# Performance work log

Measured on AMD Instinct MI355X. Metric: run time of the kernel, lower is better.

Reference implementation:

```python
import jax, jax.numpy as jnp
import numpy as np

NUM_HEADS = 8


def setup_inputs() -> dict:
    key = jax.random.key(0)
    ks = jax.random.split(key, 9)
    B, S, E = 16, 2048, 768
    s = 0.02
    return {
        "features": jax.random.normal(ks[0], (B, S, E), jnp.float32),
        "in_proj_w": jax.random.normal(ks[1], (3 * E, E), jnp.float32) * s,
        "in_proj_b": jnp.zeros((3 * E,), jnp.float32),
        "out_proj_w": jax.random.normal(ks[2], (E, E), jnp.float32) * s,
        "out_proj_b": jnp.zeros((E,), jnp.float32),
        "w1": jax.random.normal(ks[3], (384, E), jnp.float32) * s,
        "b1": jnp.zeros((384,), jnp.float32),
        "w2": jax.random.normal(ks[4], (1, 384), jnp.float32) * s,
        "b2": jnp.zeros((1,), jnp.float32),
    }


def reference(features, in_proj_w, in_proj_b, out_proj_w, out_proj_b, w1, b1, w2, b2):
    # torch nn.MultiheadAttention default batch_first=False: dim 0 is the
    # attended sequence axis (length B here), dim 1 is the MHA batch (S).
    B, S, E = features.shape
    H = NUM_HEADS
    Dh = E // H
    qkv = features @ in_proj_w.T + in_proj_b          # (B, S, 3E)
    q, k, v = jnp.split(qkv, 3, axis=-1)
    q = q.reshape(B, S, H, Dh)
    k = k.reshape(B, S, H, Dh)
    v = v.reshape(B, S, H, Dh)
    scale = 1.0 / jnp.sqrt(jnp.asarray(Dh, features.dtype))
    # attention over axis-0 positions (l, m in 0..B-1), per (s, h)
    scores = jnp.einsum('lshd,mshd->shlm', q * scale, k)
    attn = jax.nn.softmax(scores, axis=-1)
    ctx = jnp.einsum('shlm,mshd->lshd', attn, v).reshape(B, S, E)
    attn_out = ctx @ out_proj_w.T + out_proj_b        # (B, S, E)
    # batched 2-layer MLP (replaces the Python per-row loop)
    h = jax.nn.relu(attn_out @ w1.T + b1)             # (B, S, 384)
    prob = h @ w2.T + b2                              # (B, S, 1)
    contacts = jnp.broadcast_to(prob, (B, S, S))      # contacts[:, i, :] = prob[:, i]
    return contacts
```

## Files before the change

### kernel.cpp

```cpp
#include <hip/hip_runtime.h>

typedef unsigned short u16;
typedef __attribute__((ext_vector_type(8))) __bf16 bf16x8;
typedef __attribute__((ext_vector_type(4))) float floatx4;

#define B_DIM  16
#define S_DIM  2048
#define E_DIM  768
#define HEADS  8
#define DHEAD  96
#define MROWS  32768
#define QKV_LD 2304
#define ATT_ST 392

__device__ __forceinline__ u16 f2b(float f) {
    unsigned u = __float_as_uint(f);
    u += 0x7fffu + ((u >> 16) & 1u);
    return (u16)(u >> 16);
}
__device__ __forceinline__ float blo(unsigned u) { return __uint_as_float(u << 16); }
__device__ __forceinline__ float bhi(unsigned u) { return __uint_as_float(u & 0xffff0000u); }

__device__ __forceinline__ void axpy8(float* acc, float p, uint4 v) {
    acc[0] += p * blo(v.x); acc[1] += p * bhi(v.x);
    acc[2] += p * blo(v.y); acc[3] += p * bhi(v.y);
    acc[4] += p * blo(v.z); acc[5] += p * bhi(v.z);
    acc[6] += p * blo(v.w); acc[7] += p * bhi(v.w);
}

__global__ __launch_bounds__(256) void cvt_bf16(const float* __restrict__ in,
                                                u16* __restrict__ out, int n4) {
    int i = blockIdx.x * 256 + threadIdx.x;
    if (i < n4) {
        float4 f = ((const float4*)in)[i];
        ushort4 r;
        r.x = f2b(f.x); r.y = f2b(f.y); r.z = f2b(f.z); r.w = f2b(f.w);
        ((ushort4*)out)[i] = r;
    }
}

__global__ __launch_bounds__(256) void transpose_cvt(const float* __restrict__ in,
                                                     u16* __restrict__ out) {
    __shared__ float t[32][33];
    const int tx = threadIdx.x & 31, ty = threadIdx.x >> 5;
    int x = blockIdx.x * 32 + tx;
    int y = blockIdx.y * 32 + ty;
#pragma unroll
    for (int j = 0; j < 4; j++) t[ty + j * 8][tx] = in[(long)(y + j * 8) * 768 + x];
    __syncthreads();
    x = blockIdx.y * 32 + tx;
    y = blockIdx.x * 32 + ty;
#pragma unroll
    for (int j = 0; j < 4; j++) out[(long)(y + j * 8) * 768 + x] = f2b(t[tx][ty + j * 8]);
}

__global__ __launch_bounds__(256) void cbias_kernel(const float* __restrict__ w1,
                                                    const float* __restrict__ bo,
                                                    const float* __restrict__ b1,
                                                    float* __restrict__ c) {
    __shared__ float red[4];
    const int n = blockIdx.x, tid = threadIdx.x;
    const float* row = w1 + (long)n * 768;
    float s = row[tid] * bo[tid] + row[tid + 256] * bo[tid + 256] + row[tid + 512] * bo[tid + 512];
#pragma unroll
    for (int off = 32; off > 0; off >>= 1) s += __shfl_xor(s, off);
    if ((tid & 63) == 0) red[tid >> 6] = s;
    __syncthreads();
    if (tid == 0) c[n] = red[0] + red[1] + red[2] + red[3] + b1[n];
}

template<bool OUTF32, bool PERM, bool SWIZ>
__global__ __launch_bounds__(256) void gemm_bt(const u16* __restrict__ A, int lda,
                                               const u16* __restrict__ W,
                                               const float* __restrict__ bias,
                                               void* __restrict__ Cout, int ldc,
                                               int N, int K) {
    __shared__ __align__(16) u16 sA[128 * 32];
    __shared__ __align__(16) u16 sB[128 * 32];
    const int tid  = threadIdx.x;
    int bn, bm;
    if (SWIZ) {
        const int bx = blockIdx.x;
        bn = bx >> 8;
        bm = ((bx & 7) << 5) | ((bx >> 3) & 31);
    } else {
        bn = blockIdx.x;
        bm = blockIdx.y;
    }
    const int lane = tid & 63;
    const int wid  = tid >> 6;
    const int wm   = (wid >> 1) * 64;
    const int wn   = (wid & 1) * 64;
    const int ar = tid >> 2;
    const int ac = (tid & 3) * 8;
    const u16* Ap = A + (long)(bm * 128 + ar) * lda + ac;
    const u16* Wp = W + (long)(bn * 128 + ar) * K + ac;
    const long a2 = (long)64 * lda;
    const long w2 = (long)64 * K;

    floatx4 acc[4][4] = {};
    const int fr = lane & 15;
    const int fq = (lane >> 4) * 8;

    for (int k0 = 0; k0 < K; k0 += 32) {
        __builtin_amdgcn_global_load_lds((const __attribute__((address_space(1))) void*)(Ap + k0),
                                         (__attribute__((address_space(3))) void*)(sA + tid * 8), 16, 0, 0);
        __builtin_amdgcn_global_load_lds((const __attribute__((address_space(1))) void*)(Ap + a2 + k0),
                                         (__attribute__((address_space(3))) void*)(sA + 2048 + tid * 8), 16, 0, 0);
        __builtin_amdgcn_global_load_lds((const __attribute__((address_space(1))) void*)(Wp + k0),
                                         (__attribute__((address_space(3))) void*)(sB + tid * 8), 16, 0, 0);
        __builtin_amdgcn_global_load_lds((const __attribute__((address_space(1))) void*)(Wp + w2 + k0),
                                         (__attribute__((address_space(3))) void*)(sB + 2048 + tid * 8), 16, 0, 0);
        __syncthreads();

        bf16x8 aF[4], bF[4];
#pragma unroll
        for (int i = 0; i < 4; i++) {
            aF[i] = *(const bf16x8*)(sA + (wm + i * 16 + fr) * 32 + fq);
            bF[i] = *(const bf16x8*)(sB + (wn + i * 16 + fr) * 32 + fq);
        }
#pragma unroll
        for (int i = 0; i < 4; i++)
#pragma unroll
            for (int j = 0; j < 4; j++)
                acc[i][j] = __builtin_amdgcn_mfma_f32_16x16x32_bf16(aF[i], bF[j], acc[i][j], 0, 0, 0);
        __syncthreads();
    }

    const int rq = (lane >> 4) * 4;
#pragma unroll
    for (int i = 0; i < 4; i++) {
#pragma unroll
        for (int j = 0; j < 4; j++) {
            const int row0 = bm * 128 + wm + i * 16 + rq;
            const int col  = bn * 128 + wn + j * 16 + fr;
            const float bv = bias[col];
#pragma unroll
            for (int r = 0; r < 4; r++) {
                float v = acc[i][j][r] + bv;
                const int rl = row0 + r;
                const long grow = PERM ? (long)(((rl & 2047) << 4) | (rl >> 11)) : (long)rl;
                if (OUTF32) ((float*)Cout)[grow * ldc + col] = v;
                else        ((u16*)Cout)[grow * ldc + col]   = f2b(v);
            }
        }
    }
}

__global__ __launch_bounds__(256) void attn_kernel(u16* __restrict__ qkv) {
    __shared__ __align__(16) u16 sQ[16 * ATT_ST], sK[16 * ATT_ST], sV[16 * ATT_ST];
    __shared__ float sS[4][16][16];
    const int tid = threadIdx.x;
    const int s  = blockIdx.x >> 1;
    const int hh = blockIdx.x & 1;
    const u16* base = qkv + (long)s * 16 * QKV_LD + hh * 384;

#pragma unroll
    for (int it = 0; it < 9; it++) {
        const int i = it * 256 + tid;
        const int t = i / 768, rem = i % 768, l = rem / 48, c = rem % 48;
        const u16* src = base + (long)l * QKV_LD + t * E_DIM + c * 8;
        u16* dst = (t == 0 ? sQ : t == 1 ? sK : sV) + l * ATT_ST + c * 8;
        *(uint4*)dst = *(const uint4*)src;
    }
    __syncthreads();

    const int lane = tid & 63;
    const int w    = tid >> 6;
    const int fr   = lane & 15;
    const int fq   = (lane >> 4) * 8;
    floatx4 acc = {};
    const u16* qrow = sQ + fr * ATT_ST + w * DHEAD + fq;
    const u16* krow = sK + fr * ATT_ST + w * DHEAD + fq;
#pragma unroll
    for (int st = 0; st < 3; st++) {
        bf16x8 qa = *(const bf16x8*)(qrow + st * 32);
        bf16x8 kb = *(const bf16x8*)(krow + st * 32);
        acc = __builtin_amdgcn_mfma_f32_16x16x32_bf16(qa, kb, acc, 0, 0, 0);
    }
    const int rq = (lane >> 4) * 4;
#pragma unroll
    for (int r = 0; r < 4; r++) {
        float sc = acc[r] * 0.10206207261596577f;
        float mx = sc;
#pragma unroll
        for (int off = 8; off > 0; off >>= 1) mx = fmaxf(mx, __shfl_xor(mx, off));
        float e = __expf(sc - mx);
        float sum = e;
#pragma unroll
        for (int off = 8; off > 0; off >>= 1) sum += __shfl_xor(sum, off);
        sS[w][rq + r][fr] = e / sum;
    }
    __syncthreads();

#pragma unroll
    for (int j = 0; j < 3; j++) {
        const int task = j * 256 + tid;
        const int h = task / 192, rem = task % 192, ll = rem / 12, c = rem % 12;
        float a[8] = {};
#pragma unroll
        for (int mm = 0; mm < 16; mm++) {
            const float p = sS[h][ll][mm];
            uint4 vw = *(const uint4*)(sV + mm * ATT_ST + h * DHEAD + c * 8);
            axpy8(a, p, vw);
        }
        ushort4 o0, o1;
        o0.x = f2b(a[0]); o0.y = f2b(a[1]); o0.z = f2b(a[2]); o0.w = f2b(a[3]);
        o1.x = f2b(a[4]); o1.y = f2b(a[5]); o1.z = f2b(a[6]); o1.w = f2b(a[7]);
        u16* dst = qkv + ((long)s * 16 + ll) * QKV_LD + (hh * 4 + h) * DHEAD + c * 8;
        *(ushort4*)dst = o0;
        *(ushort4*)(dst + 4) = o1;
    }
}

__global__ __launch_bounds__(256) void mlp_gemm(const u16* __restrict__ A, int lda,
                                                const u16* __restrict__ G,
                                                const float* __restrict__ cbias,
                                                const float* __restrict__ w2,
                                                float* __restrict__ part) {
    __shared__ __align__(16) u16 sA[128 * 32];
    __shared__ __align__(16) u16 sB[128 * 32];
    __shared__ float rowsum[128];
    const int tid = threadIdx.x;
    const int bm  = blockIdx.x / 3;
    const int bn  = blockIdx.x % 3;
    if (tid < 128) rowsum[tid] = 0.f;
    const int lane = tid & 63;
    const int wid  = tid >> 6;
    const int wm   = (wid >> 1) * 64;
    const int wn   = (wid & 1) * 64;
    const int ar = tid >> 2;
    const int ac = (tid & 3) * 8;
    const u16* Ap = A + (long)(bm * 128 + ar) * lda + ac;
    const u16* Wp = G + (long)(bn * 128 + ar) * 768 + ac;
    const long a2 = (long)64 * lda;
    const int fr = lane & 15;
    const int fq = (lane >> 4) * 8;
    const int rq = (lane >> 4) * 4;

    floatx4 acc[4][4] = {};
    for (int k0 = 0; k0 < 768; k0 += 32) {
        __builtin_amdgcn_global_load_lds((const __attribute__((address_space(1))) void*)(Ap + k0),
                                         (__attribute__((address_space(3))) void*)(sA + tid * 8), 16, 0, 0);
        __builtin_amdgcn_global_load_lds((const __attribute__((address_space(1))) void*)(Ap + a2 + k0),
                                         (__attribute__((address_space(3))) void*)(sA + 2048 + tid * 8), 16, 0, 0);
        __builtin_amdgcn_global_load_lds((const __attribute__((address_space(1))) void*)(Wp + k0),
                                         (__attribute__((address_space(3))) void*)(sB + tid * 8), 16, 0, 0);
        __builtin_amdgcn_global_load_lds((const __attribute__((address_space(1))) void*)(Wp + (long)64 * 768 + k0),
                                         (__attribute__((address_space(3))) void*)(sB + 2048 + tid * 8), 16, 0, 0);
        __syncthreads();
        bf16x8 aF[4], bF[4];
#pragma unroll
        for (int i = 0; i < 4; i++) {
            aF[i] = *(const bf16x8*)(sA + (wm + i * 16 + fr) * 32 + fq);
            bF[i] = *(const bf16x8*)(sB + (wn + i * 16 + fr) * 32 + fq);
        }
#pragma unroll
        for (int i = 0; i < 4; i++)
#pragma unroll
            for (int j = 0; j < 4; j++)
                acc[i][j] = __builtin_amdgcn_mfma_f32_16x16x32_bf16(aF[i], bF[j], acc[i][j], 0, 0, 0);
        __syncthreads();
    }
    float partl[4][4] = {};
#pragma unroll
    for (int j = 0; j < 4; j++) {
        const int col = bn * 128 + wn + j * 16 + fr;
        const float cv = cbias[col];
        const float wv = w2[col];
#pragma unroll
        for (int i = 0; i < 4; i++)
#pragma unroll
            for (int r = 0; r < 4; r++)
                partl[i][r] += fmaxf(acc[i][j][r] + cv, 0.f) * wv;
    }
#pragma unroll
    for (int i = 0; i < 4; i++)
#pragma unroll
        for (int r = 0; r < 4; r++) {
            float v = partl[i][r];
#pragma unroll
            for (int off = 8; off > 0; off >>= 1) v += __shfl_xor(v, off);
            if (fr == 0) atomicAdd(&rowsum[wm + i * 16 + rq + r], v);
        }
    __syncthreads();
    if (tid < 128) part[(long)bn * MROWS + bm * 128 + tid] = rowsum[tid];
}

__global__ __launch_bounds__(256) void bcast_kernel(const float* __restrict__ part,
                                                    const float* __restrict__ b2,
                                                    float* __restrict__ out) {
    const int tid = threadIdx.x;
    const long p0 = (long)blockIdx.x * 4;
    const float b2v = b2[0];
#pragma unroll
    for (int r = 0; r < 4; r++) {
        const long p = p0 + r;
        const float pv = part[p] + part[MROWS + p] + part[2 * MROWS + p] + b2v;
        float4* dst = (float4*)(out + ((p & 15) * S_DIM + (p >> 4)) * S_DIM);
        float4 v4 = make_float4(pv, pv, pv, pv);
        dst[tid] = v4;
        dst[tid + 256] = v4;
    }
}

extern "C" void kernel_launch(void* const* d_in, const int* in_sizes, int n_in,
                              void* d_out, int out_size, void* d_ws, size_t ws_size,
                              hipStream_t stream) {
    const float* features   = (const float*)d_in[0];
    const float* in_proj_b  = (const float*)d_in[2];
    const float* out_proj_b = (const float*)d_in[4];
    const float* b1 = (const float*)d_in[6];
    const float* w2 = (const float*)d_in[7];
    const float* b2 = (const float*)d_in[8];
    float* out = (float*)d_out;

    char* p = (char*)d_ws;
    u16* fbf = (u16*)p; p += (size_t)MROWS * E_DIM * 2;
    u16* wib = (u16*)p; p += (size_t)QKV_LD * E_DIM * 2;
    u16* w1b = (u16*)p; p += (size_t)384 * E_DIM * 2;
    u16* WoT = (u16*)p; p += (size_t)E_DIM * E_DIM * 2;
    u16* Gbf = (u16*)p; p += (size_t)384 * E_DIM * 2;
    float* cbuf  = (float*)p; p += 384 * 4;
    float* partb = (float*)p; p += (size_t)3 * MROWS * 4;
    float* zeros = (float*)p; p += 768 * 4;
    p = (char*)(((size_t)p + 255) & ~(size_t)255);
    u16* qkv = (u16*)p; p += (size_t)MROWS * QKV_LD * 2;
    u16* ctx = qkv;

    hipMemsetAsync(zeros, 0, 768 * 4, stream);

    cvt_bf16<<<(MROWS * E_DIM / 4 + 255) / 256, 256, 0, stream>>>(features, fbf, MROWS * E_DIM / 4);
    cvt_bf16<<<(QKV_LD * E_DIM / 4 + 255) / 256, 256, 0, stream>>>((const float*)d_in[1], wib, QKV_LD * E_DIM / 4);
    cvt_bf16<<<(384 * E_DIM / 4 + 255) / 256, 256, 0, stream>>>((const float*)d_in[5], w1b, 384 * E_DIM / 4);
    transpose_cvt<<<dim3(24, 24), 256, 0, stream>>>((const float*)d_in[3], WoT);
    cbias_kernel<<<384, 256, 0, stream>>>((const float*)d_in[5], out_proj_b, b1, cbuf);

    gemm_bt<false, false, false><<<dim3(6, 3), 256, 0, stream>>>(
        w1b, E_DIM, WoT, zeros, Gbf, E_DIM, E_DIM, E_DIM);
    gemm_bt<false, true, true><<<dim3(4608), 256, 0, stream>>>(
        fbf, E_DIM, wib, in_proj_b, qkv, QKV_LD, QKV_LD, E_DIM);
    attn_kernel<<<S_DIM * 2, 256, 0, stream>>>(qkv);
    mlp_gemm<<<768, 256, 0, stream>>>(ctx, QKV_LD, Gbf, cbuf, w2, partb);
    bcast_kernel<<<MROWS / 4, 256, 0, stream>>>(partb, b2, out);
}
```

Measured before the change: 622.1 us.

## Fuse prep kernels, stage GEMM epilogue through LDS, remap block swizzle

Merges the three bf16 conversions, the weight transpose and the bias-fold reduction into one launch, and drops the zero-buffer memset by passing a null bias. The GEMM epilogue now writes bf16 results to a shared tile and stores 16-byte vectors per row, replacing scattered 2-byte stores that the permuted QKV layout made strided. The QKV GEMM block-to-tile mapping is also changed so that blocks on the same XCD share an A/B tile region for better L2 reuse. The costs are extra LDS and barriers in the epilogue, plus per-block branching in the fused prep kernel.

```diff
diff --git a/kernel.cpp b/kernel.cpp
--- a/kernel.cpp
+++ b/kernel.cpp
@@ -28,61 +28,75 @@
     acc[6] += p * blo(v.w); acc[7] += p * bhi(v.w);
 }
 
-__global__ __launch_bounds__(256) void cvt_bf16(const float* __restrict__ in,
-                                                u16* __restrict__ out, int n4) {
-    int i = blockIdx.x * 256 + threadIdx.x;
-    if (i < n4) {
-        float4 f = ((const float4*)in)[i];
+#define PB0 24576
+#define PB1 26304
+#define PB2 26592
+#define PB3 27168
+#define PB4 27552
+__global__ __launch_bounds__(256) void prep(const float* __restrict__ features,
+                                            const float* __restrict__ in_proj_w,
+                                            const float* __restrict__ w1,
+                                            const float* __restrict__ out_proj_w,
+                                            const float* __restrict__ bo,
+                                            const float* __restrict__ b1,
+                                            u16* __restrict__ fbf, u16* __restrict__ wib,
+                                            u16* __restrict__ w1b, u16* __restrict__ WoT,
+                                            float* __restrict__ cbuf) {
+    __shared__ float tsh[32][33];
+    const int b = blockIdx.x, tid = threadIdx.x;
+    if (b < PB2) {
+        const float* src; u16* dst; long i;
+        if (b < PB0)      { src = features;  dst = fbf; i = (long)b * 256 + tid; }
+        else if (b < PB1) { src = in_proj_w; dst = wib; i = (long)(b - PB0) * 256 + tid; }
+        else              { src = w1;        dst = w1b; i = (long)(b - PB1) * 256 + tid; }
+        float4 f = ((const float4*)src)[i];
         ushort4 r;
         r.x = f2b(f.x); r.y = f2b(f.y); r.z = f2b(f.z); r.w = f2b(f.w);
-        ((ushort4*)out)[i] = r;
-    }
-}
-
-__global__ __launch_bounds__(256) void transpose_cvt(const float* __restrict__ in,
-                                                     u16* __restrict__ out) {
-    __shared__ float t[32][33];
-    const int tx = threadIdx.x & 31, ty = threadIdx.x >> 5;
-    int x = blockIdx.x * 32 + tx;
-    int y = blockIdx.y * 32 + ty;
-#pragma unroll
-    for (int j = 0; j < 4; j++) t[ty + j * 8][tx] = in[(long)(y + j * 8) * 768 + x];
-    __syncthreads();
-    x = blockIdx.y * 32 + tx;
-    y = blockIdx.x * 32 + ty;
-#pragma unroll
-    for (int j = 0; j < 4; j++) out[(long)(y + j * 8) * 768 + x] = f2b(t[tx][ty + j * 8]);
-}
-
-__global__ __launch_bounds__(256) void cbias_kernel(const float* __restrict__ w1,
-                                                    const float* __restrict__ bo,
-                                                    const float* __restrict__ b1,
-                                                    float* __restrict__ c) {
-    __shared__ float red[4];
-    const int n = blockIdx.x, tid = threadIdx.x;
-    const float* row = w1 + (long)n * 768;
-    float s = row[tid] * bo[tid] + row[tid + 256] * bo[tid + 256] + row[tid + 512] * bo[tid + 512];
-#pragma unroll
-    for (int off = 32; off > 0; off >>= 1) s += __shfl_xor(s, off);
-    if ((tid & 63) == 0) red[tid >> 6] = s;
-    __syncthreads();
-    if (tid == 0) c[n] = red[0] + red[1] + red[2] + red[3] + b1[n];
-}
-
-template<bool OUTF32, bool PERM, bool SWIZ>
+        ((ushort4*)dst)[i] = r;
+    } else if (b < PB3) {
+        const int t = b - PB2;
+        const int bxT = t % 24, byT = t / 24;
+        const int tx = tid & 31, ty = tid >> 5;
+        int x = bxT * 32 + tx;
+        int y = byT * 32 + ty;
+#pragma unroll
+        for (int j = 0; j < 4; j++) tsh[ty + j * 8][tx] = out_proj_w[(long)(y + j * 8) * 768 + x];
+        __syncthreads();
+        x = byT * 32 + tx;
+        y = bxT * 32 + ty;
+#pragma unroll
+        for (int j = 0; j < 4; j++) WoT[(long)(y + j * 8) * 768 + x] = f2b(tsh[tx][ty + j * 8]);
+    } else {
+        const int n = b - PB3;
+        const float* row = w1 + (long)n * 768;
+        float s = row[tid] * bo[tid] + row[tid + 256] * bo[tid + 256] + row[tid + 512] * bo[tid + 512];
+#pragma unroll
+        for (int off = 32; off > 0; off >>= 1) s += __shfl_xor(s, off);
+        if ((tid & 63) == 0) tsh[0][tid >> 6] = s;
+        __syncthreads();
+        if (tid == 0) cbuf[n] = tsh[0][0] + tsh[0][1] + tsh[0][2] + tsh[0][3] + b1[n];
+    }
+}
+
+template<bool PERM, bool SWIZ>
 __global__ __launch_bounds__(256) void gemm_bt(const u16* __restrict__ A, int lda,
                                                const u16* __restrict__ W,
                                                const float* __restrict__ bias,
-                                               void* __restrict__ Cout, int ldc,
+                                               u16* __restrict__ Cout, int ldc,
                                                int N, int K) {
     __shared__ __align__(16) u16 sA[128 * 32];
     __shared__ __align__(16) u16 sB[128 * 32];
+    __shared__ __align__(16) u16 sC[32 * 132];
     const int tid  = threadIdx.x;
     int bn, bm;
     if (SWIZ) {
-        const int bx = blockIdx.x;
-        bn = bx >> 8;
-        bm = ((bx & 7) << 5) | ((bx >> 3) & 31);
+        const int bx  = blockIdx.x;
+        const int xcd = bx & 7;
+        const int q   = bx >> 3;
+        const int s   = q / 144;
+        const int r   = q % 144;
+        bn = r >> 3;
+        bm = s * 64 + xcd * 8 + (r & 7);
     } else {
         bn = blockIdx.x;
         bm = blockIdx.y;
@@ -128,22 +142,36 @@
     }
 
     const int rq = (lane >> 4) * 4;
-#pragma unroll
-    for (int i = 0; i < 4; i++) {
-#pragma unroll
-        for (int j = 0; j < 4; j++) {
-            const int row0 = bm * 128 + wm + i * 16 + rq;
-            const int col  = bn * 128 + wn + j * 16 + fr;
-            const float bv = bias[col];
-#pragma unroll
-            for (int r = 0; r < 4; r++) {
-                float v = acc[i][j][r] + bv;
-                const int rl = row0 + r;
-                const long grow = PERM ? (long)(((rl & 2047) << 4) | (rl >> 11)) : (long)rl;
-                if (OUTF32) ((float*)Cout)[grow * ldc + col] = v;
-                else        ((u16*)Cout)[grow * ldc + col]   = f2b(v);
+    float bvj[4];
+#pragma unroll
+    for (int j = 0; j < 4; j++)
+        bvj[j] = bias ? bias[bn * 128 + wn + j * 16 + fr] : 0.f;
+#pragma unroll
+    for (int p = 0; p < 4; p++) {
+        if ((p >> 1) == (wid >> 1)) {
+#pragma unroll
+            for (int ii = 0; ii < 2; ii++) {
+                const int i = (p & 1) * 2 + ii;
+#pragma unroll
+                for (int j = 0; j < 4; j++) {
+                    const int col = wn + j * 16 + fr;
+#pragma unroll
+                    for (int r = 0; r < 4; r++)
+                        sC[(ii * 16 + rq + r) * 132 + col] = f2b(acc[i][j][r] + bvj[j]);
+                }
             }
         }
+        __syncthreads();
+#pragma unroll
+        for (int q2 = 0; q2 < 2; q2++) {
+            const int lr = (tid >> 4) + q2 * 16;
+            const int c  = tid & 15;
+            uint4 v = *(const uint4*)(sC + lr * 132 + c * 8);
+            const int rl = bm * 128 + p * 32 + lr;
+            const long grow = PERM ? (long)(((rl & 2047) << 4) | (rl >> 11)) : (long)rl;
+            *(uint4*)(Cout + grow * ldc + bn * 128 + c * 8) = v;
+        }
+        __syncthreads();
     }
 }
 
@@ -323,22 +351,16 @@
     u16* Gbf = (u16*)p; p += (size_t)384 * E_DIM * 2;
     float* cbuf  = (float*)p; p += 384 * 4;
     float* partb = (float*)p; p += (size_t)3 * MROWS * 4;
-    float* zeros = (float*)p; p += 768 * 4;
     p = (char*)(((size_t)p + 255) & ~(size_t)255);
     u16* qkv = (u16*)p; p += (size_t)MROWS * QKV_LD * 2;
     u16* ctx = qkv;
 
-    hipMemsetAsync(zeros, 0, 768 * 4, stream);
-
-    cvt_bf16<<<(MROWS * E_DIM / 4 + 255) / 256, 256, 0, stream>>>(features, fbf, MROWS * E_DIM / 4);
-    cvt_bf16<<<(QKV_LD * E_DIM / 4 + 255) / 256, 256, 0, stream>>>((const float*)d_in[1], wib, QKV_LD * E_DIM / 4);
-    cvt_bf16<<<(384 * E_DIM / 4 + 255) / 256, 256, 0, stream>>>((const float*)d_in[5], w1b, 384 * E_DIM / 4);
-    transpose_cvt<<<dim3(24, 24), 256, 0, stream>>>((const float*)d_in[3], WoT);
-    cbias_kernel<<<384, 256, 0, stream>>>((const float*)d_in[5], out_proj_b, b1, cbuf);
-
-    gemm_bt<false, false, false><<<dim3(6, 3), 256, 0, stream>>>(
-        w1b, E_DIM, WoT, zeros, Gbf, E_DIM, E_DIM, E_DIM);
-    gemm_bt<false, true, true><<<dim3(4608), 256, 0, stream>>>(
+    prep<<<PB4, 256, 0, stream>>>(features, (const float*)d_in[1], (const float*)d_in[5],
+                                  (const float*)d_in[3], out_proj_b, b1,
+                                  fbf, wib, w1b, WoT, cbuf);
+    gemm_bt<false, false><<<dim3(6, 3), 256, 0, stream>>>(
+        w1b, E_DIM, WoT, nullptr, Gbf, E_DIM, E_DIM, E_DIM);
+    gemm_bt<true, true><<<dim3(4608), 256, 0, stream>>>(
         fbf, E_DIM, wib, in_proj_b, qkv, QKV_LD, QKV_LD, E_DIM);
     attn_kernel<<<S_DIM * 2, 256, 0, stream>>>(qkv);
     mlp_gemm<<<768, 256, 0, stream>>>(ctx, QKV_LD, Gbf, cbuf, w2, partb);
```

New measurement: 606.1 us. -2.6%, faster.
